# Optimization experiments

Hardware: AMD Instinct MI355X
Metric: run time of the kernel (lower is better)

The kernel has to match this reference:

```python
import jax, jax.numpy as jnp
import numpy as np

_SAMPLING_EPS = 1e-05
_FP16_TINY = float(np.finfo(np.float16).tiny)  # masked_fill value used by the torch code


def _token_mask(tokens, num_seqs, vocab_size):
    # bin-count via scatter-add into width vocab+1 (padding id == vocab), then mask
    rows = jnp.arange(num_seqs)[:, None]
    counts = jnp.zeros((num_seqs, vocab_size + 1), jnp.int32).at[rows, tokens].add(1)
    return counts[:, :vocab_size] > 0


def setup_inputs() -> dict:
    key = jax.random.key(0)
    ks = jax.random.split(key, 9)
    B, V, PL, OL = 128, 128000, 2048, 256
    logits = jax.random.normal(ks[0], (B, V), dtype=jnp.float32) * 4.0
    prompt_tokens = jax.random.randint(ks[1], (B, PL), 0, V, dtype=jnp.int64)
    output_tokens = jax.random.randint(ks[2], (B, OL), 0, V, dtype=jnp.int64)
    presence_penalties = jax.random.uniform(ks[3], (B,), dtype=jnp.float32)
    frequency_penalties = jax.random.uniform(ks[4], (B,), dtype=jnp.float32)
    repetition_penalties = 1.0 + 0.3 * jax.random.uniform(ks[5], (B,), dtype=jnp.float32)
    temperature = 0.1 + 0.9 * jax.random.uniform(ks[6], (B,), dtype=jnp.float32)
    top_k = jax.random.randint(ks[7], (B,), 1, 100, dtype=jnp.int64)
    top_p = 0.5 + 0.49 * jax.random.uniform(ks[8], (B,), dtype=jnp.float32)
    return {
        "logits": logits,
        "prompt_tokens": prompt_tokens,
        "output_tokens": output_tokens,
        "presence_penalties": presence_penalties,
        "frequency_penalties": frequency_penalties,
        "repetition_penalties": repetition_penalties,
        "temperature": temperature,
        "top_k": top_k,
        "top_p": top_p,
    }


def reference(logits, prompt_tokens, output_tokens, presence_penalties,
              frequency_penalties, repetition_penalties, temperature,
              top_k, top_p):
    B, V = logits.shape
    logits = logits.astype(jnp.float32)

    # --- penalties (NOTE: torch code computes frequency counts but never applies
    # frequency_penalties; we faithfully do the same) ---
    prompt_mask = _token_mask(prompt_tokens, B, V)
    output_mask = _token_mask(output_tokens, B, V)
    pen = jnp.where(prompt_mask | output_mask, repetition_penalties[:, None], 1.0)
    logits = jnp.where(logits > 0, logits / pen, logits * pen)
    logits = logits - presence_penalties[:, None] * output_mask.astype(jnp.float32)

    # --- temperature ---
    temp = jnp.where(temperature < _SAMPLING_EPS, 1.0, temperature)
    logits = logits / temp[:, None]

    # --- top-k / top-p via ascending sort (mirrors torch implementation) ---
    idx = jnp.argsort(logits, axis=-1)                      # ascending
    ls = jnp.take_along_axis(logits, idx, axis=-1)
    thr_pos = (V - top_k.astype(jnp.int32))[:, None]
    thr = jnp.take_along_axis(ls, thr_pos, axis=-1)         # [B,1]
    ls = jnp.where(ls < thr, _FP16_TINY, ls)
    probs_sort = jax.nn.softmax(ls, axis=-1)
    csum = jnp.cumsum(probs_sort, axis=-1)
    tp_mask = csum <= (1.0 - top_p)[:, None]
    tp_mask = tp_mask.at[:, -1].set(False)
    ls = jnp.where(tp_mask, _FP16_TINY, ls)

    # unsort back to original vocab order
    rows = jnp.arange(B)[:, None]
    out_logits = jnp.zeros_like(logits).at[rows, idx].set(ls)

    probs = jax.nn.softmax(out_logits, axis=-1)
    return probs, prompt_mask, output_mask
```

## Files before the change

### kernel.cpp

```cpp
#include <hip/hip_runtime.h>
#include <math.h>

#define B   128
#define V   128000
#define WPR 4000
#define PL  2048
#define OL  256
#define BPR 25
#define ITERS 5
#define TLOC 128
#define CAP  6144
#define FP16_TINY 6.103515625e-05f

__device__ __forceinline__ unsigned key_of(float f) {
    unsigned u = __float_as_uint(f);
    unsigned m = (unsigned)(((int)u) >> 31) | 0x80000000u;
    return u ^ m;
}
__device__ __forceinline__ float key_inv(unsigned k) {
    unsigned u = (k & 0x80000000u) ? (k ^ 0x80000000u) : ~k;
    return __uint_as_float(u);
}

__device__ __forceinline__ float xform(float x, int pm, int om,
                                       float rep, float pres, float temp) {
#pragma clang fp contract(off)
    float pen = (pm | om) ? rep : 1.0f;
    float l = (x > 0.0f) ? (x / pen) : (x * pen);
    if (om) l = l - pres;
    return l / temp;
}

__global__ __launch_bounds__(256) void k_zero(unsigned* __restrict__ p, int n) {
    int i = blockIdx.x * 256 + threadIdx.x;
    int stride = gridDim.x * 256;
    for (; i < n; i += stride) p[i] = 0u;
}

__global__ __launch_bounds__(256) void k_scatter(const int* __restrict__ ptok,
                                                 const int* __restrict__ otok,
                                                 unsigned* __restrict__ bitP,
                                                 unsigned* __restrict__ bitO) {
    int i = blockIdx.x * 256 + threadIdx.x;
    int np = B * PL;
    int total = np + B * OL;
    if (i >= total) return;
    if (i < np) {
        int r = i >> 11;
        int t = ptok[i];
        if ((unsigned)t < (unsigned)V)
            atomicOr(&bitP[r * WPR + (t >> 5)], 1u << (t & 31));
    } else {
        int j = i - np;
        int r = j >> 8;
        int t = otok[j];
        if ((unsigned)t < (unsigned)V)
            atomicOr(&bitO[r * WPR + (t >> 5)], 1u << (t & 31));
    }
}

__global__ __launch_bounds__(256) void k_main(
    const float* __restrict__ logits,
    const unsigned* __restrict__ bitP, const unsigned* __restrict__ bitO,
    const float* __restrict__ rep, const float* __restrict__ pres,
    const float* __restrict__ temp,
    float* __restrict__ outPm, float* __restrict__ outOm,
    unsigned* __restrict__ cnt, unsigned long long* __restrict__ cand)
{
    __shared__ unsigned h[4096];
    __shared__ unsigned sA[256];
    __shared__ int s_beta;
    __shared__ unsigned s_base;
    int r = blockIdx.y;
    int c0 = blockIdx.x * (ITERS * 1024);
    int t = threadIdx.x;
    for (int i = t; i < 4096; i += 256) h[i] = 0u;
    __syncthreads();
    float rp = rep[r], pp = pres[r];
    float tt = temp[r]; tt = (tt < 1e-5f) ? 1.0f : tt;
    const float* lrow = logits + (size_t)r * V;
    float* pmrow = outPm + (size_t)r * V;
    float* omrow = outOm + (size_t)r * V;
    const unsigned* bp = bitP + r * WPR;
    const unsigned* bo = bitO + r * WPR;
    float4 lv[ITERS];
#pragma unroll
    for (int it = 0; it < ITERS; it++) {
        int i = c0 + it * 1024 + t * 4;
        float4 x = *(const float4*)(lrow + i);
        unsigned wp = bp[i >> 5], wo = bo[i >> 5];
        int sh = i & 31;
        float xs[4] = {x.x, x.y, x.z, x.w};
        float res[4], fp[4], fo[4];
#pragma unroll
        for (int j = 0; j < 4; j++) {
            int p = (wp >> (sh + j)) & 1;
            int o = (wo >> (sh + j)) & 1;
            float l = xform(xs[j], p, o, rp, pp, tt);
            atomicAdd(&h[key_of(l) >> 20], 1u);
            res[j] = l; fp[j] = (float)p; fo[j] = (float)o;
        }
        lv[it] = make_float4(res[0], res[1], res[2], res[3]);
        *(float4*)(pmrow + i) = make_float4(fp[0], fp[1], fp[2], fp[3]);
        *(float4*)(omrow + i) = make_float4(fo[0], fo[1], fo[2], fo[3]);
    }
    __syncthreads();
    unsigned cs = 0;
#pragma unroll
    for (int j = 0; j < 16; j++) cs += h[t * 16 + j];
    sA[t] = cs;
    __syncthreads();
    unsigned v = cs;
    for (int st = 1; st < 256; st <<= 1) {
        unsigned add = (t + st < 256) ? sA[t + st] : 0u;
        __syncthreads();
        v += add; sA[t] = v;
        __syncthreads();
    }
    unsigned Snext = (t < 255) ? sA[t + 1] : 0u;
    if (sA[t] >= TLOC && Snext < TLOC) {
        unsigned run = Snext;
        int beta = t * 16;
        for (int j = 15; j >= 0; j--) {
            run += h[t * 16 + j];
            if (run >= TLOC) { beta = t * 16 + j; break; }
        }
        s_beta = beta;
    }
    __syncthreads();
    unsigned beta = (unsigned)s_beta;
    unsigned myc = 0;
#pragma unroll
    for (int it = 0; it < ITERS; it++) {
        float xs[4] = {lv[it].x, lv[it].y, lv[it].z, lv[it].w};
#pragma unroll
        for (int j = 0; j < 4; j++)
            if ((key_of(xs[j]) >> 20) >= beta) myc++;
    }
    sA[t] = myc;
    __syncthreads();
    unsigned pv = myc;
    for (int st = 1; st < 256; st <<= 1) {
        unsigned add = (t >= st) ? sA[t - st] : 0u;
        __syncthreads();
        pv += add; sA[t] = pv;
        __syncthreads();
    }
    if (t == 255) s_base = atomicAdd(&cnt[r], pv);
    __syncthreads();
    unsigned w = s_base + (pv - myc);
#pragma unroll
    for (int it = 0; it < ITERS; it++) {
        float xs[4] = {lv[it].x, lv[it].y, lv[it].z, lv[it].w};
#pragma unroll
        for (int j = 0; j < 4; j++) {
            unsigned key = key_of(xs[j]);
            if ((key >> 20) >= beta) {
                if (w < (unsigned)CAP) {
                    int idx = c0 + it * 1024 + t * 4 + j;
                    cand[(size_t)r * CAP + w] =
                        ((unsigned long long)key << 32) | (unsigned)idx;
                }
                w++;
            }
        }
    }
}

__global__ __launch_bounds__(256) void k_select(
    const unsigned* __restrict__ cnt, const unsigned long long* __restrict__ cand,
    const int* __restrict__ topk, const float* __restrict__ topp,
    float4* __restrict__ params, int* __restrict__ idxc)
{
    __shared__ unsigned rh[256];
    __shared__ unsigned rsuf[256];
    __shared__ unsigned long long kv[256];
    __shared__ unsigned s_prefix, s_krem, s_kcnt;
    int r = blockIdx.x;
    int t = threadIdx.x;
    int n = (int)min(cnt[r], (unsigned)CAP);
    const unsigned long long* crow = cand + (size_t)r * CAP;
    int k = topk[r]; k = max(1, min(k, 127));
    if (t == 0) { s_prefix = 0u; s_krem = (unsigned)k; }
    __syncthreads();
    for (int round = 3; round >= 0; round--) {
        int shift = round * 8;
        unsigned prefix = s_prefix;
        unsigned krem = s_krem;
        unsigned maskAbove = (round == 3) ? 0u : (0xFFFFFFFFu << (shift + 8));
        rh[t] = 0u;
        __syncthreads();
        for (int i = t; i < n; i += 256) {
            unsigned key = (unsigned)(crow[i] >> 32);
            if ((key & maskAbove) == (prefix & maskAbove))
                atomicAdd(&rh[(key >> shift) & 255u], 1u);
        }
        __syncthreads();
        unsigned vv = rh[t];
        rsuf[t] = vv;
        __syncthreads();
        for (int st = 1; st < 256; st <<= 1) {
            unsigned add = (t + st < 256) ? rsuf[t + st] : 0u;
            __syncthreads();
            vv += add; rsuf[t] = vv;
            __syncthreads();
        }
        unsigned Sx = (t < 255) ? rsuf[t + 1] : 0u;
        if (rsuf[t] >= krem && Sx < krem) {
            s_prefix = prefix | ((unsigned)t << shift);
            s_krem = krem - Sx;
        }
        __syncthreads();
    }
    unsigned thrkey = s_prefix;
    if (t == 0) s_kcnt = 0u;
    __syncthreads();
    for (int i = t; i < n; i += 256) {
        if ((unsigned)(crow[i] >> 32) >= thrkey) {
            unsigned pos = atomicAdd(&s_kcnt, 1u);
            if (pos < 256u) kv[pos] = crow[i];
        }
    }
    __syncthreads();
    int K = (int)min(s_kcnt, 256u);
    if (t >= K) kv[t] = 0ULL;
    __syncthreads();
    for (unsigned k2 = 2; k2 <= 256; k2 <<= 1) {
        for (unsigned j2 = k2 >> 1; j2 > 0; j2 >>= 1) {
            unsigned ixj = (unsigned)t ^ j2;
            if (ixj > (unsigned)t) {
                unsigned long long a = kv[t], b = kv[ixj];
                bool descBlock = (((unsigned)t & k2) == 0u);
                bool doSwap = descBlock ? (a < b) : (a > b);
                if (doSwap) { kv[t] = b; kv[ixj] = a; }
            }
            __syncthreads();
        }
    }
    if (t == 0) {
        float Mxf = key_inv((unsigned)(kv[0] >> 32));
        double MxD = (double)Mxf;
        double e_tinyD = exp((double)FP16_TINY - MxD);
        double S = 0.0;
        for (int i = K - 1; i >= 0; i--)
            S += exp((double)key_inv((unsigned)(kv[i] >> 32)) - MxD);
        double Z1 = (double)(V - K) * e_tinyD + S;
        double base = (double)(V - K) * e_tinyD / Z1;
        double thresh = 1.0 - (double)topp[r];
        double dd = base;
        int ns = K;
        for (int a = 0; a <= K - 2; a++) {
            int i = K - 1 - a;
            dd += exp((double)key_inv((unsigned)(kv[i] >> 32)) - MxD) / Z1;
            if (dd <= thresh) ns--;
        }
        unsigned bkey = (unsigned)(kv[ns - 1] >> 32);
        float v_b = key_inv(bkey);
        unsigned idx_cut = (unsigned)(kv[ns - 1] & 0xFFFFFFFFu);
        float tiny_e = expf(FP16_TINY - Mxf);
        double S2 = 0.0;
        for (int i = 0; i < ns; i++)
            S2 += (double)expf(key_inv((unsigned)(kv[i] >> 32)) - Mxf);
        double Z2 = (double)(V - ns) * (double)tiny_e + S2;
        float invZ2 = (float)(1.0 / Z2);
        params[r] = make_float4(v_b, Mxf, invZ2, tiny_e * invZ2);
        idxc[r] = (int)idx_cut;
    }
}

__global__ __launch_bounds__(256) void k_final(
    const float* __restrict__ logits,
    const unsigned* __restrict__ bitP, const unsigned* __restrict__ bitO,
    const float* __restrict__ rep, const float* __restrict__ pres,
    const float* __restrict__ temp,
    const float4* __restrict__ params, const int* __restrict__ idxc,
    float* __restrict__ probs)
{
    int r = blockIdx.y;
    int c0 = blockIdx.x * (ITERS * 1024);
    int t = threadIdx.x;
    float rp = rep[r], pp = pres[r];
    float tt = temp[r]; tt = (tt < 1e-5f) ? 1.0f : tt;
    float4 pr = params[r];
    float v_b = pr.x, Mx = pr.y, invZ2 = pr.z, ptiny = pr.w;
    unsigned idx_cut = (unsigned)idxc[r];
    const float* lrow = logits + (size_t)r * V;
    float* orow = probs + (size_t)r * V;
    const unsigned* bp = bitP + r * WPR;
    const unsigned* bo = bitO + r * WPR;
#pragma unroll
    for (int it = 0; it < ITERS; it++) {
        int i = c0 + it * 1024 + t * 4;
        float4 x = *(const float4*)(lrow + i);
        unsigned wp = bp[i >> 5], wo = bo[i >> 5];
        int sh = i & 31;
        float xs[4] = {x.x, x.y, x.z, x.w};
        float res[4];
#pragma unroll
        for (int j = 0; j < 4; j++) {
            int p = (wp >> (sh + j)) & 1;
            int o = (wo >> (sh + j)) & 1;
            float l = xform(xs[j], p, o, rp, pp, tt);
            bool keep = (l > v_b) || (l == v_b && (unsigned)(i + j) >= idx_cut);
            res[j] = keep ? (expf(l - Mx) * invZ2) : ptiny;
        }
        *(float4*)(orow + i) = make_float4(res[0], res[1], res[2], res[3]);
    }
}

extern "C" void kernel_launch(void* const* d_in, const int* in_sizes, int n_in,
                              void* d_out, int out_size, void* d_ws, size_t ws_size,
                              hipStream_t stream) {
    const float* logits = (const float*)d_in[0];
    const int* ptok     = (const int*)d_in[1];
    const int* otok     = (const int*)d_in[2];
    const float* pres   = (const float*)d_in[3];
    const float* rep    = (const float*)d_in[5];
    const float* temp   = (const float*)d_in[6];
    const int* topk     = (const int*)d_in[7];
    const float* topp   = (const float*)d_in[8];

    float* out_probs = (float*)d_out;
    float* out_pm = out_probs + (size_t)B * V;
    float* out_om = out_pm + (size_t)B * V;

    unsigned* ws0 = (unsigned*)d_ws;
    float4* params = (float4*)d_ws;
    int* idxc = (int*)(ws0 + 512);
    unsigned* bitP = ws0 + 768;
    unsigned* bitO = bitP + B * WPR;
    unsigned* cnt  = bitO + B * WPR;
    unsigned long long* cand =
        (unsigned long long*)(cnt + B + 64);

    k_zero<<<256, 256, 0, stream>>>(bitP, 2 * B * WPR + B);

    int ntok = B * PL + B * OL;
    k_scatter<<<(ntok + 255) / 256, 256, 0, stream>>>(ptok, otok, bitP, bitO);

    dim3 g(BPR, B);
    k_main<<<g, 256, 0, stream>>>(logits, bitP, bitO, rep, pres, temp,
                                  out_pm, out_om, cnt, cand);
    k_select<<<B, 256, 0, stream>>>(cnt, cand, topk, topp, params, idxc);
    k_final<<<g, 256, 0, stream>>>(logits, bitP, bitO, rep, pres, temp,
                                   params, idxc, out_probs);
}
```

Before: 342.5 us.

## Parallelize top-p selection reductions, stage candidates in LDS, use nontemporal stores

The select kernel now copies the candidate list into shared memory once instead of rereading global memory in each radix round. The serial single-thread exp/sum and top-p scan become block-wide parallel reductions and a suffix scan. Output and mask writes switch to nontemporal stores to reduce cache pollution on streaming writes. Summation order changes (the S2 sum now uses double exp instead of expf), which could slightly alter numerics at the cutoff boundary, and the 48KB+ of LDS may limit occupancy of the 128-block select kernel.

```diff
diff --git a/kernel.cpp b/kernel.cpp
--- a/kernel.cpp
+++ b/kernel.cpp
@@ -11,6 +11,12 @@
 #define TLOC 128
 #define CAP  6144
 #define FP16_TINY 6.103515625e-05f
+
+typedef float f4_nt __attribute__((ext_vector_type(4)));
+__device__ __forceinline__ void nt_store4(float* p, float a, float b, float c, float d) {
+    f4_nt v = {a, b, c, d};
+    __builtin_nontemporal_store(v, (f4_nt*)p);
+}
 
 __device__ __forceinline__ unsigned key_of(float f) {
     unsigned u = __float_as_uint(f);
@@ -101,8 +107,8 @@
             res[j] = l; fp[j] = (float)p; fo[j] = (float)o;
         }
         lv[it] = make_float4(res[0], res[1], res[2], res[3]);
-        *(float4*)(pmrow + i) = make_float4(fp[0], fp[1], fp[2], fp[3]);
-        *(float4*)(omrow + i) = make_float4(fo[0], fo[1], fo[2], fo[3]);
+        nt_store4(pmrow + i, fp[0], fp[1], fp[2], fp[3]);
+        nt_store4(omrow + i, fo[0], fo[1], fo[2], fo[3]);
     }
     __syncthreads();
     unsigned cs = 0;
@@ -172,14 +178,17 @@
     const int* __restrict__ topk, const float* __restrict__ topp,
     float4* __restrict__ params, int* __restrict__ idxc)
 {
+    __shared__ unsigned long long list[CAP];
+    __shared__ unsigned long long kv[256];
     __shared__ unsigned rh[256];
     __shared__ unsigned rsuf[256];
-    __shared__ unsigned long long kv[256];
+    __shared__ double sD[256];
     __shared__ unsigned s_prefix, s_krem, s_kcnt;
     int r = blockIdx.x;
     int t = threadIdx.x;
     int n = (int)min(cnt[r], (unsigned)CAP);
     const unsigned long long* crow = cand + (size_t)r * CAP;
+    for (int i = t; i < n; i += 256) list[i] = crow[i];
     int k = topk[r]; k = max(1, min(k, 127));
     if (t == 0) { s_prefix = 0u; s_krem = (unsigned)k; }
     __syncthreads();
@@ -191,7 +200,7 @@
         rh[t] = 0u;
         __syncthreads();
         for (int i = t; i < n; i += 256) {
-            unsigned key = (unsigned)(crow[i] >> 32);
+            unsigned key = (unsigned)(list[i] >> 32);
             if ((key & maskAbove) == (prefix & maskAbove))
                 atomicAdd(&rh[(key >> shift) & 255u], 1u);
         }
@@ -216,9 +225,9 @@
     if (t == 0) s_kcnt = 0u;
     __syncthreads();
     for (int i = t; i < n; i += 256) {
-        if ((unsigned)(crow[i] >> 32) >= thrkey) {
+        if ((unsigned)(list[i] >> 32) >= thrkey) {
             unsigned pos = atomicAdd(&s_kcnt, 1u);
-            if (pos < 256u) kv[pos] = crow[i];
+            if (pos < 256u) kv[pos] = list[i];
         }
     }
     __syncthreads();
@@ -237,30 +246,53 @@
             __syncthreads();
         }
     }
+    float Mxf = key_inv((unsigned)(kv[0] >> 32));
+    double MxD = (double)Mxf;
+    double e_t = (t < K) ? exp((double)key_inv((unsigned)(kv[t] >> 32)) - MxD)
+                         : 0.0;
+    sD[t] = e_t;
+    __syncthreads();
+    for (int st = 128; st > 0; st >>= 1) {
+        if (t < st) sD[t] += sD[t + st];
+        __syncthreads();
+    }
+    double S = sD[0];
+    __syncthreads();
+    double e_tinyD = exp((double)FP16_TINY - MxD);
+    double Z1 = (double)(V - K) * e_tinyD + S;
+    double base = (double)(V - K) * e_tinyD / Z1;
+    double thresh = 1.0 - (double)topp[r];
+    sD[t] = e_t;
+    __syncthreads();
+    double sv = e_t;
+    for (int st = 1; st < 256; st <<= 1) {
+        double add = (t + st < 256) ? sD[t + st] : 0.0;
+        __syncthreads();
+        sv += add; sD[t] = sv;
+        __syncthreads();
+    }
+    double suf_t = sv;
+    unsigned flag = (t >= 1 && t < K && (base + suf_t / Z1) <= thresh) ? 1u : 0u;
+    rsuf[t] = flag;
+    __syncthreads();
+    for (int st = 128; st > 0; st >>= 1) {
+        if (t < st) rsuf[t] += rsuf[t + st];
+        __syncthreads();
+    }
+    int cm = (int)rsuf[0];
+    int ns = K - cm;
+    sD[t] = (t < ns) ? e_t : 0.0;
+    __syncthreads();
+    for (int st = 128; st > 0; st >>= 1) {
+        if (t < st) sD[t] += sD[t + st];
+        __syncthreads();
+    }
     if (t == 0) {
-        float Mxf = key_inv((unsigned)(kv[0] >> 32));
-        double MxD = (double)Mxf;
-        double e_tinyD = exp((double)FP16_TINY - MxD);
-        double S = 0.0;
-        for (int i = K - 1; i >= 0; i--)
-            S += exp((double)key_inv((unsigned)(kv[i] >> 32)) - MxD);
-        double Z1 = (double)(V - K) * e_tinyD + S;
-        double base = (double)(V - K) * e_tinyD / Z1;
-        double thresh = 1.0 - (double)topp[r];
-        double dd = base;
-        int ns = K;
-        for (int a = 0; a <= K - 2; a++) {
-            int i = K - 1 - a;
-            dd += exp((double)key_inv((unsigned)(kv[i] >> 32)) - MxD) / Z1;
-            if (dd <= thresh) ns--;
-        }
+        double S2 = sD[0];
         unsigned bkey = (unsigned)(kv[ns - 1] >> 32);
         float v_b = key_inv(bkey);
         unsigned idx_cut = (unsigned)(kv[ns - 1] & 0xFFFFFFFFu);
         float tiny_e = expf(FP16_TINY - Mxf);
-        double S2 = 0.0;
-        for (int i = 0; i < ns; i++)
-            S2 += (double)expf(key_inv((unsigned)(kv[i] >> 32)) - Mxf);
         double Z2 = (double)(V - ns) * (double)tiny_e + S2;
         float invZ2 = (float)(1.0 / Z2);
         params[r] = make_float4(v_b, Mxf, invZ2, tiny_e * invZ2);
@@ -304,7 +336,7 @@
             bool keep = (l > v_b) || (l == v_b && (unsigned)(i + j) >= idx_cut);
             res[j] = keep ? (expf(l - Mx) * invZ2) : ptiny;
         }
-        *(float4*)(orow + i) = make_float4(res[0], res[1], res[2], res[3]);
+        nt_store4(orow + i, res[0], res[1], res[2], res[3]);
     }
 }
 
```

Result: faster. 319.7 us (-6.7%).
